# Kernel tuning notes

Hardware: AMD Instinct MI355X
Metric: run time of the kernel (lower is better)

The kernel has to match this reference:

```python
import jax, jax.numpy as jnp
import numpy as np

NEG_BIG = 1e13  # matches the torch module's (mask-1)*1e13 additive mask


def setup_inputs() -> dict:
    key = jax.random.key(0)
    k1, k2, k3, k4 = jax.random.split(key, 4)
    B, Lq, Lk, D = 32, 1024, 1024, 1024  # D = 2*hidden = 2*embedding
    query = jax.random.normal(k1, (B, Lq, D), dtype=jnp.float32)
    key_t = jax.random.normal(k2, (B, Lk, D), dtype=jnp.float32)
    key_mask = jax.random.randint(k3, (B, Lk), 0, 2).astype(jnp.float32)
    # Linear(hidden*2 -> embedding*2): weight [out, in] torch convention
    W = jax.random.normal(k4, (D, D), dtype=jnp.float32) * (1.0 / np.sqrt(D))
    b = jnp.zeros((D,), dtype=jnp.float32)
    return {"query": query, "key": key_t, "key_mask": key_mask, "W": W, "b": b}


def reference(query, key, key_mask, W, b):
    # query_emb: Dropout (identity at eval) -> Linear -> ReLU
    query_feat = jax.nn.relu(jnp.einsum("bqd,ed->bqe", query, W) + b)  # [B,Lq,D]
    # bmm with multiplicatively masked key
    masked_key = key * key_mask[:, :, None]                             # [B,Lk,D]
    score = jnp.einsum("bqd,bkd->bqk", query_feat, masked_key)          # [B,Lq,Lk]
    # masked_softmax: score*mask + (mask-1)*1e13, softmax over last dim
    m = key_mask[:, None, :]                                            # [B,1,Lk]
    attn = jax.nn.softmax(score * m + (m - 1.0) * NEG_BIG, axis=-1)     # [B,Lq,Lk]
    # weighted sum over the UNmasked key (as in the original module)
    return jnp.einsum("bqk,bkd->bqd", attn, key)                        # [B,Lq,D]
```

## Files before the change

### kernel.cpp

```cpp
#include <hip/hip_runtime.h>
#include <hip/hip_bf16.h>


typedef __attribute__((ext_vector_type(4))) float f32x4;
typedef __attribute__((ext_vector_type(8))) short s16x8;

#define MFMA16(a, b, c) __builtin_amdgcn_mfma_f32_16x16x32_bf16((a), (b), (c), 0, 0, 0)

__device__ __forceinline__ unsigned short f2bf(float x) {
  unsigned u = __builtin_bit_cast(unsigned, x);
  return (unsigned short)((u + 0x7FFFu + ((u >> 16) & 1u)) >> 16);
}
__device__ __forceinline__ float bf2f(unsigned short h) {
  return __builtin_bit_cast(float, ((unsigned)h) << 16);
}
__device__ __forceinline__ int swz(int row, int col) {
  return (row * 64 + col) ^ ((row & 7) << 3);
}
__device__ __forceinline__ void cvt8(const float* __restrict__ s, s16x8& h8, s16x8& l8) {
  f32x4 a = *(const f32x4*)s;
  f32x4 b = *(const f32x4*)(s + 4);
#pragma unroll
  for (int i = 0; i < 8; i++) {
    float v = (i < 4) ? a[i] : b[i - 4];
    unsigned short hu = f2bf(v);
    unsigned short lu = f2bf(v - bf2f(hu));
    h8[i] = (short)hu;
    l8[i] = (short)lu;
  }
}
__device__ __forceinline__ void gld16(const void* g, void* lds) {
  __builtin_amdgcn_global_load_lds((const __attribute__((address_space(1))) unsigned int*)g,
                                   (__attribute__((address_space(3))) unsigned int*)lds, 16, 0, 0);
}

#define OFF_KHI 0ULL
#define OFF_KLO 67108864ULL
#define OFF_KHIT 134217728ULL
#define OFF_QHI 201326592ULL
#define OFF_QLO 268435456ULL
#define OFF_WHI 335544320ULL
#define OFF_WLO 337641472ULL
#define WS_TIER_A 339738624ULL
#define QA_LO 33554432ULL

__global__ __launch_bounds__(256) void k_cvt_qw(const float* __restrict__ Q,
                                                unsigned short* __restrict__ Qhi,
                                                unsigned short* __restrict__ Qlo,
                                                const float* __restrict__ W,
                                                unsigned short* __restrict__ Whi,
                                                unsigned short* __restrict__ Wlo) {
  int i = blockIdx.x * 256 + threadIdx.x;
  s16x8 h, l;
  if (i < 4194304) {
    cvt8(Q + (size_t)i * 8, h, l);
    *(s16x8*)(Qhi + (size_t)i * 8) = h;
    *(s16x8*)(Qlo + (size_t)i * 8) = l;
  } else {
    int j = i - 4194304;
    if (j < 131072) {
      cvt8(W + (size_t)j * 8, h, l);
      *(s16x8*)(Whi + (size_t)j * 8) = h;
      *(s16x8*)(Wlo + (size_t)j * 8) = l;
    }
  }
}

__global__ __launch_bounds__(256) void k_cvt_k(const float* __restrict__ K,
                                               unsigned short* __restrict__ Khi,
                                               unsigned short* __restrict__ Klo,
                                               unsigned short* __restrict__ KhiT) {
  __shared__ unsigned T[64 * 65];
  const int t = threadIdx.x;
  const int db0 = blockIdx.x * 64, kb0 = blockIdx.y * 64, b = blockIdx.z;
  const size_t base = (size_t)b * 1024 * 1024;
#pragma unroll
  for (int i = 0; i < 2; i++) {
    const int r = (t >> 3) + i * 32, c0 = (t & 7) * 8;
    s16x8 h, l;
    cvt8(K + base + (size_t)(kb0 + r) * 1024 + db0 + c0, h, l);
    *(s16x8*)(Khi + base + (size_t)(kb0 + r) * 1024 + db0 + c0) = h;
    *(s16x8*)(Klo + base + (size_t)(kb0 + r) * 1024 + db0 + c0) = l;
#pragma unroll
    for (int j = 0; j < 8; j++)
      T[r * 65 + c0 + j] = ((unsigned)(unsigned short)h[j] << 16) | (unsigned short)l[j];
  }
  __syncthreads();
#pragma unroll
  for (int i = 0; i < 2; i++) {
    const int rd = (t >> 3) + i * 32, ck0 = (t & 7) * 8;
    s16x8 h;
#pragma unroll
    for (int j = 0; j < 8; j++) h[j] = (short)(unsigned short)(T[(ck0 + j) * 65 + rd] >> 16);
    *(s16x8*)(KhiT + base + (size_t)(db0 + rd) * 1024 + kb0 + ck0) = h;
  }
}

__global__ __launch_bounds__(256, 2) void k_qf2(const unsigned short* __restrict__ Qhi,
                                                const unsigned short* __restrict__ Qlo,
                                                const unsigned short* __restrict__ Whi,
                                                const unsigned short* __restrict__ Wlo,
                                                const float* __restrict__ bias,
                                                float* __restrict__ outp) {
  __shared__ __align__(16) unsigned short Ah[128 * 64], Al[128 * 64], Bh[128 * 64], Bl[128 * 64];
  const int t = threadIdx.x;
  const int i = blockIdx.x + blockIdx.y * 256;
  const int x = i & 7, j = i >> 3;
  const int n0 = (j & 7) * 128;
  const int m0 = (x * 32 + (j >> 3)) * 128;
  const int w = t >> 6, l = t & 63, wm = w >> 1, wn = w & 1, g = l >> 4, ln = l & 15;
  const int lrow = l >> 3, lc8 = (l & 7) * 8;
  const f32x4 fz = {0.f, 0.f, 0.f, 0.f};
  f32x4 acc[4][4];
#pragma unroll
  for (int a = 0; a < 4; a++)
#pragma unroll
    for (int bq = 0; bq < 4; bq++) acc[a][bq] = fz;
#pragma unroll 1
  for (int k0 = 0; k0 < 1024; k0 += 64) {
#pragma unroll
    for (int jj = 0; jj < 4; jj++) {
      const int ch = w * 4 + jj;
      const int row = ch * 8 + lrow;
      const int sc = lc8 ^ (lrow << 3);
      gld16(Qhi + (size_t)(m0 + row) * 1024 + k0 + sc, &Ah[ch * 512]);
      gld16(Qlo + (size_t)(m0 + row) * 1024 + k0 + sc, &Al[ch * 512]);
      gld16(Whi + (size_t)(n0 + row) * 1024 + k0 + sc, &Bh[ch * 512]);
      gld16(Wlo + (size_t)(n0 + row) * 1024 + k0 + sc, &Bl[ch * 512]);
    }
    __syncthreads();
#pragma unroll
    for (int ks = 0; ks < 2; ks++) {
      const int kc = ks * 32 + g * 8;
      s16x8 ah[4], al[4], bh[4], bl[4];
#pragma unroll
      for (int mf = 0; mf < 4; mf++) {
        const int row = wm * 64 + mf * 16 + ln;
        const int idx = row * 64 + (kc ^ ((row & 7) << 3));
        ah[mf] = *(const s16x8*)&Ah[idx];
        al[mf] = *(const s16x8*)&Al[idx];
      }
#pragma unroll
      for (int nf = 0; nf < 4; nf++) {
        const int row = wn * 64 + nf * 16 + ln;
        const int idx = row * 64 + (kc ^ ((row & 7) << 3));
        bh[nf] = *(const s16x8*)&Bh[idx];
        bl[nf] = *(const s16x8*)&Bl[idx];
      }
#pragma unroll
      for (int mf = 0; mf < 4; mf++)
#pragma unroll
        for (int nf = 0; nf < 4; nf++) {
          acc[mf][nf] = MFMA16(ah[mf], bh[nf], acc[mf][nf]);
          acc[mf][nf] = MFMA16(ah[mf], bl[nf], acc[mf][nf]);
          acc[mf][nf] = MFMA16(al[mf], bh[nf], acc[mf][nf]);
        }
    }
    __syncthreads();
  }
  unsigned short* qA = (unsigned short*)outp;
#pragma unroll
  for (int nf = 0; nf < 4; nf++) {
    const int c = n0 + wn * 64 + nf * 16 + ln;
    const float bv = bias[c];
    const int kchunk = c >> 5, lhib = ((c >> 3) & 3) << 4, jj = c & 7;
#pragma unroll
    for (int mf = 0; mf < 4; mf++)
#pragma unroll
      for (int r = 0; r < 4; r++) {
        const int R = m0 + wm * 64 + mf * 16 + g * 4 + r;
        float v = acc[mf][nf][r] + bv;
        v = v > 0.f ? v : 0.f;
        unsigned short h = f2bf(v);
        const size_t fo = (((size_t)(R >> 4) * 32 + kchunk) * 64 + ((R & 15) + lhib)) * 8 + jj;
        qA[fo] = h;
        qA[QA_LO + fo] = f2bf(v - bf2f(h));
      }
  }
}

__global__ __launch_bounds__(512, 2) void k_attn2(const unsigned short* __restrict__ Khi,
                                                  const unsigned short* __restrict__ Klo,
                                                  const float* __restrict__ mask,
                                                  const unsigned short* __restrict__ qA,
                                                  unsigned short* __restrict__ attnw) {
  __shared__ __align__(16) unsigned short kbuf[2][2][128 * 64];
  __shared__ float mask_s[1024];
  __shared__ float red[4][64];
  const int t = threadIdx.x;
  const int i = blockIdx.y * 16 + blockIdx.x;
  const int x = i & 7, jj = i >> 3;
  const int b = x * 4 + (jj >> 4), qt = jj & 15;
  const int q0 = qt * 64;
  const int w = t >> 6, l = t & 63, wm = w >> 2, wn = w & 3, g = l >> 4, ln = l & 15;
  const int lrow = l >> 3, lc8 = (l & 7) * 8, sc = lc8 ^ (lrow << 3);
  for (int ii = t; ii < 1024; ii += 512) mask_s[ii] = mask[b * 1024 + ii];
  const f32x4 fz = {0.f, 0.f, 0.f, 0.f};
  f32x4 acc[8][2][2];
#pragma unroll
  for (int kt = 0; kt < 8; kt++)
#pragma unroll
    for (int mf = 0; mf < 2; mf++)
#pragma unroll
      for (int nf = 0; nf < 2; nf++) acc[kt][mf][nf] = fz;
  const size_t kbase = (size_t)b * 1024 * 1024;
  const int qblk0 = (b * 1024 + q0) >> 4;

  auto stageK = [&](int buf, int kt, int dc) {
#pragma unroll
    for (int jj2 = 0; jj2 < 2; jj2++) {
      const int ch = w * 2 + jj2;
      const int row = ch * 8 + lrow;
      const size_t go = kbase + (size_t)(kt * 128 + row) * 1024 + dc * 64 + sc;
      gld16(Khi + go, &kbuf[buf][0][ch * 512]);
      gld16(Klo + go, &kbuf[buf][1][ch * 512]);
    }
  };

  stageK(0, 0, 0);
  __syncthreads();
#pragma unroll 1
  for (int dc = 0; dc < 16; dc++) {
    s16x8 qh[2][2], ql[2][2];
#pragma unroll
    for (int mf = 0; mf < 2; mf++) {
      const int qb = qblk0 + wm * 2 + mf;
#pragma unroll
      for (int ks = 0; ks < 2; ks++) {
        const size_t fo = (((size_t)qb * 32 + dc * 2 + ks) * 64 + l) * 8;
        qh[mf][ks] = *(const s16x8*)(qA + fo);
        ql[mf][ks] = *(const s16x8*)(qA + QA_LO + fo);
      }
    }
#pragma unroll
    for (int kt = 0; kt < 8; kt++) {
      const int snum = dc * 8 + kt;
      if (snum == 127) {
        asm volatile("s_waitcnt vmcnt(0)" ::: "memory");
      } else if (kt == 0) {
        asm volatile("s_waitcnt vmcnt(8)" ::: "memory");
      } else {
        asm volatile("s_waitcnt vmcnt(4)" ::: "memory");
      }
      __builtin_amdgcn_s_barrier();
      __builtin_amdgcn_sched_barrier(0);
      if (snum < 127) {
        const int nkt = (kt + 1) & 7;
        const int ndc = (kt == 7) ? dc + 1 : dc;
        stageK((snum + 1) & 1, nkt, ndc);
      }
      const int cur = snum & 1;
      __builtin_amdgcn_s_setprio(1);
#pragma unroll
      for (int ks = 0; ks < 2; ks++) {
        const int kc = ks * 32 + g * 8;
        s16x8 bh[2], bl[2];
#pragma unroll
        for (int nf = 0; nf < 2; nf++) {
          const int row = wn * 32 + nf * 16 + ln;
          const int idx = row * 64 + (kc ^ ((row & 7) << 3));
          bh[nf] = *(const s16x8*)&kbuf[cur][0][idx];
          bl[nf] = *(const s16x8*)&kbuf[cur][1][idx];
        }
#pragma unroll
        for (int mf = 0; mf < 2; mf++)
#pragma unroll
          for (int nf = 0; nf < 2; nf++) {
            acc[kt][mf][nf] = MFMA16(qh[mf][ks], bh[nf], acc[kt][mf][nf]);
            acc[kt][mf][nf] = MFMA16(qh[mf][ks], bl[nf], acc[kt][mf][nf]);
            acc[kt][mf][nf] = MFMA16(ql[mf][ks], bh[nf], acc[kt][mf][nf]);
          }
      }
      __builtin_amdgcn_s_setprio(0);
    }
  }
  __syncthreads();
  float rmax[2][4];
#pragma unroll
  for (int mf = 0; mf < 2; mf++)
#pragma unroll
    for (int r = 0; r < 4; r++) rmax[mf][r] = -1e30f;
#pragma unroll
  for (int kt = 0; kt < 8; kt++)
#pragma unroll
    for (int nf = 0; nf < 2; nf++) {
      const int k = kt * 128 + wn * 32 + nf * 16 + ln;
      const bool mk = mask_s[k] != 0.f;
#pragma unroll
      for (int mf = 0; mf < 2; mf++)
#pragma unroll
        for (int r = 0; r < 4; r++)
          if (mk) rmax[mf][r] = fmaxf(rmax[mf][r], acc[kt][mf][nf][r]);
    }
#pragma unroll
  for (int off = 1; off < 16; off <<= 1)
#pragma unroll
    for (int mf = 0; mf < 2; mf++)
#pragma unroll
      for (int r = 0; r < 4; r++) rmax[mf][r] = fmaxf(rmax[mf][r], __shfl_xor(rmax[mf][r], off));
  if (ln == 0) {
#pragma unroll
    for (int mf = 0; mf < 2; mf++)
#pragma unroll
      for (int r = 0; r < 4; r++) red[wn][wm * 32 + mf * 16 + g * 4 + r] = rmax[mf][r];
  }
  __syncthreads();
#pragma unroll
  for (int mf = 0; mf < 2; mf++)
#pragma unroll
    for (int r = 0; r < 4; r++) {
      const int row = wm * 32 + mf * 16 + g * 4 + r;
      rmax[mf][r] = fmaxf(fmaxf(red[0][row], red[1][row]), fmaxf(red[2][row], red[3][row]));
    }
  __syncthreads();
  float rsum[2][4];
#pragma unroll
  for (int mf = 0; mf < 2; mf++)
#pragma unroll
    for (int r = 0; r < 4; r++) rsum[mf][r] = 0.f;
#pragma unroll
  for (int kt = 0; kt < 8; kt++)
#pragma unroll
    for (int nf = 0; nf < 2; nf++) {
      const int k = kt * 128 + wn * 32 + nf * 16 + ln;
      const bool mk = mask_s[k] != 0.f;
#pragma unroll
      for (int mf = 0; mf < 2; mf++)
#pragma unroll
        for (int r = 0; r < 4; r++)
          if (mk) rsum[mf][r] += __expf(acc[kt][mf][nf][r] - rmax[mf][r]);
    }
#pragma unroll
  for (int off = 1; off < 16; off <<= 1)
#pragma unroll
    for (int mf = 0; mf < 2; mf++)
#pragma unroll
      for (int r = 0; r < 4; r++) rsum[mf][r] += __shfl_xor(rsum[mf][r], off);
  if (ln == 0) {
#pragma unroll
    for (int mf = 0; mf < 2; mf++)
#pragma unroll
      for (int r = 0; r < 4; r++) red[wn][wm * 32 + mf * 16 + g * 4 + r] = rsum[mf][r];
  }
  __syncthreads();
  float rinv[2][4];
#pragma unroll
  for (int mf = 0; mf < 2; mf++)
#pragma unroll
    for (int r = 0; r < 4; r++) {
      const int row = wm * 32 + mf * 16 + g * 4 + r;
      rinv[mf][r] = 1.f / (red[0][row] + red[1][row] + red[2][row] + red[3][row]);
    }
#pragma unroll
  for (int kt = 0; kt < 8; kt++)
#pragma unroll
    for (int nf = 0; nf < 2; nf++) {
      const int k = kt * 128 + wn * 32 + nf * 16 + ln;
      const bool mk = mask_s[k] != 0.f;
#pragma unroll
      for (int mf = 0; mf < 2; mf++)
#pragma unroll
        for (int r = 0; r < 4; r++) {
          const int q = q0 + wm * 32 + mf * 16 + g * 4 + r;
          float p = mk ? __expf(acc[kt][mf][nf][r] - rmax[mf][r]) * rinv[mf][r] : 0.f;
          attnw[(size_t)(b * 1024 + q) * 1024 + k] = f2bf(p);
        }
    }
}

__global__ __launch_bounds__(512, 1) void k_pv2(const unsigned short* __restrict__ KhiT,
                                                const unsigned short* __restrict__ attnw,
                                                float* __restrict__ dout) {
  __shared__ __align__(16) unsigned short Pb[2][128 * 64];
  __shared__ __align__(16) unsigned short KTb[2][512 * 64];
  const int t = threadIdx.x;
  const int i = blockIdx.y * 8 + blockIdx.x;
  const int x = i & 7, jj = i >> 3;
  const int b = x * 4 + (jj >> 3), qt = jj & 7;
  const int q0 = qt * 128, d0 = blockIdx.z * 512;
  const int w = t >> 6, l = t & 63, wm = w >> 2, wd = w & 3, g = l >> 4, ln = l & 15;
  const int lrow = l >> 3, lc8 = (l & 7) * 8, sc = lc8 ^ (lrow << 3);
  const f32x4 fz = {0.f, 0.f, 0.f, 0.f};
  f32x4 acc[4][8];
#pragma unroll
  for (int a = 0; a < 4; a++)
#pragma unroll
    for (int bq = 0; bq < 8; bq++) acc[a][bq] = fz;
  const size_t kbase = (size_t)b * 1024 * 1024;

  auto stageP = [&](int buf, int k0) {
#pragma unroll
    for (int jj2 = 0; jj2 < 2; jj2++) {
      const int ch = w * 2 + jj2;
      const int row = ch * 8 + lrow;
      gld16(attnw + (size_t)(b * 1024 + q0 + row) * 1024 + k0 + sc, &Pb[buf][ch * 512]);
    }
  };
  auto stageKT = [&](int buf, int k0) {
#pragma unroll
    for (int jj2 = 0; jj2 < 8; jj2++) {
      const int ch = w * 8 + jj2;
      const int row = ch * 8 + lrow;
      gld16(KhiT + kbase + (size_t)(d0 + row) * 1024 + k0 + sc, &KTb[buf][ch * 512]);
    }
  };

  stageP(0, 0);
  stageKT(0, 0);
#pragma unroll 1
  for (int s = 0; s < 16; s++) {
    asm volatile("s_waitcnt vmcnt(0)" ::: "memory");
    __builtin_amdgcn_s_barrier();
    __builtin_amdgcn_sched_barrier(0);
    if (s < 15) {
      stageP((s + 1) & 1, (s + 1) * 64);
      stageKT((s + 1) & 1, (s + 1) * 64);
    }
    const int cur = s & 1;
    __builtin_amdgcn_s_setprio(1);
#pragma unroll
    for (int ks = 0; ks < 2; ks++) {
      const int kc = ks * 32 + g * 8;
      s16x8 a[4], bb[8];
#pragma unroll
      for (int mf = 0; mf < 4; mf++) {
        const int row = wm * 64 + mf * 16 + ln;
        a[mf] = *(const s16x8*)&Pb[cur][row * 64 + (kc ^ ((row & 7) << 3))];
      }
#pragma unroll
      for (int nf = 0; nf < 8; nf++) {
        const int row = wd * 128 + nf * 16 + ln;
        bb[nf] = *(const s16x8*)&KTb[cur][row * 64 + (kc ^ ((row & 7) << 3))];
      }
#pragma unroll
      for (int mf = 0; mf < 4; mf++)
#pragma unroll
        for (int nf = 0; nf < 8; nf++) acc[mf][nf] = MFMA16(a[mf], bb[nf], acc[mf][nf]);
    }
    __builtin_amdgcn_s_setprio(0);
  }
#pragma unroll
  for (int mf = 0; mf < 4; mf++)
#pragma unroll
    for (int nf = 0; nf < 8; nf++)
#pragma unroll
      for (int r = 0; r < 4; r++) {
        const int q = q0 + wm * 64 + mf * 16 + g * 4 + r;
        const int d = d0 + wd * 128 + nf * 16 + ln;
        dout[(size_t)(b * 1024 + q) * 1024 + d] = acc[mf][nf][r];
      }
}

__global__ __launch_bounds__(256, 2) void k_qf(const float* __restrict__ Q,
                                               const float* __restrict__ W,
                                               const float* __restrict__ bias,
                                               float* __restrict__ qf) {
  __shared__ __align__(16) short Ah[128 * 64], Al[128 * 64], Bh[128 * 64], Bl[128 * 64];
  const int t = threadIdx.x;
  const int m0 = blockIdx.x * 128, n0 = blockIdx.y * 128;
  const int w = t >> 6, l = t & 63, wm = w >> 1, wn = w & 1, g = l >> 4, ln = l & 15;
  const f32x4 fz = {0.f, 0.f, 0.f, 0.f};
  f32x4 acc[4][4];
#pragma unroll
  for (int a = 0; a < 4; a++)
#pragma unroll
    for (int bq = 0; bq < 4; bq++) acc[a][bq] = fz;
  const int srow = t >> 1, scol = (t & 1) * 32;
#pragma unroll 1
  for (int k0 = 0; k0 < 1024; k0 += 64) {
    const float* sa = Q + (size_t)(m0 + srow) * 1024 + k0 + scol;
    const float* sb = W + (size_t)(n0 + srow) * 1024 + k0 + scol;
#pragma unroll
    for (int c = 0; c < 32; c += 8) {
      s16x8 h, lo;
      cvt8(sa + c, h, lo);
      int si = swz(srow, scol + c);
      *(s16x8*)&Ah[si] = h;
      *(s16x8*)&Al[si] = lo;
    }
#pragma unroll
    for (int c = 0; c < 32; c += 8) {
      s16x8 h, lo;
      cvt8(sb + c, h, lo);
      int si = swz(srow, scol + c);
      *(s16x8*)&Bh[si] = h;
      *(s16x8*)&Bl[si] = lo;
    }
    __syncthreads();
#pragma unroll
    for (int ks = 0; ks < 2; ks++) {
      const int kc = ks * 32 + g * 8;
      s16x8 ah[4], al[4], bh[4], bl[4];
#pragma unroll
      for (int mf = 0; mf < 4; mf++) {
        int si = swz(wm * 64 + mf * 16 + ln, kc);
        ah[mf] = *(s16x8*)&Ah[si];
        al[mf] = *(s16x8*)&Al[si];
      }
#pragma unroll
      for (int nf = 0; nf < 4; nf++) {
        int si = swz(wn * 64 + nf * 16 + ln, kc);
        bh[nf] = *(s16x8*)&Bh[si];
        bl[nf] = *(s16x8*)&Bl[si];
      }
#pragma unroll
      for (int mf = 0; mf < 4; mf++)
#pragma unroll
        for (int nf = 0; nf < 4; nf++) {
          acc[mf][nf] = MFMA16(ah[mf], bh[nf], acc[mf][nf]);
          acc[mf][nf] = MFMA16(ah[mf], bl[nf], acc[mf][nf]);
          acc[mf][nf] = MFMA16(al[mf], bh[nf], acc[mf][nf]);
        }
    }
    __syncthreads();
  }
#pragma unroll
  for (int nf = 0; nf < 4; nf++) {
    const int col = n0 + wn * 64 + nf * 16 + ln;
    const float bv = bias[col];
#pragma unroll
    for (int mf = 0; mf < 4; mf++)
#pragma unroll
      for (int r = 0; r < 4; r++) {
        const int row = m0 + wm * 64 + mf * 16 + g * 4 + r;
        float v = acc[mf][nf][r] + bv;
        qf[(size_t)row * 1024 + col] = v > 0.f ? v : 0.f;
      }
  }
}

__global__ __launch_bounds__(512, 2) void k_attn(const float* __restrict__ Key,
                                                 const float* __restrict__ mask,
                                                 float* __restrict__ dout) {
  __shared__ __align__(16) short qh[64 * 64], qlo[64 * 64], kh[128 * 64], klo[128 * 64];
  __shared__ float mask_s[1024];
  __shared__ float red[4][64];
  const int t = threadIdx.x;
  const int qt = blockIdx.x, b = blockIdx.y;
  const int q0 = qt * 64;
  const int w = t >> 6, l = t & 63, wm = w >> 2, wn = w & 3, g = l >> 4, ln = l & 15;
  for (int i = t; i < 1024; i += 512) mask_s[i] = mask[b * 1024 + i];
  const f32x4 fz = {0.f, 0.f, 0.f, 0.f};
  f32x4 acc[8][2][2];
#pragma unroll
  for (int kt = 0; kt < 8; kt++)
#pragma unroll
    for (int mf = 0; mf < 2; mf++)
#pragma unroll
      for (int nf = 0; nf < 2; nf++) acc[kt][mf][nf] = fz;
  const float* qfb = dout + (size_t)(b * 1024 + q0) * 1024;
  const float* kb = Key + (size_t)b * 1024 * 1024;
  const int qrow = t >> 3, qcol = (t & 7) * 8;
  const int krow = t >> 2, kcol0 = (t & 3) * 16;
#pragma unroll 1
  for (int dc = 0; dc < 16; dc++) {
    {
      s16x8 h, lo;
      cvt8(qfb + (size_t)qrow * 1024 + dc * 64 + qcol, h, lo);
      int si = swz(qrow, qcol);
      *(s16x8*)&qh[si] = h;
      *(s16x8*)&qlo[si] = lo;
    }
#pragma unroll
    for (int kt = 0; kt < 8; kt++) {
      {
        const float* s = kb + (size_t)(kt * 128 + krow) * 1024 + dc * 64 + kcol0;
        s16x8 h, lo;
        cvt8(s, h, lo);
        int si = swz(krow, kcol0);
        *(s16x8*)&kh[si] = h;
        *(s16x8*)&klo[si] = lo;
        cvt8(s + 8, h, lo);
        si = swz(krow, kcol0 + 8);
        *(s16x8*)&kh[si] = h;
        *(s16x8*)&klo[si] = lo;
      }
      __syncthreads();
#pragma unroll
      for (int ks = 0; ks < 2; ks++) {
        const int kc = ks * 32 + g * 8;
        s16x8 ah[2], al2[2], bh[2], bl[2];
#pragma unroll
        for (int mf = 0; mf < 2; mf++) {
          int si = swz(wm * 32 + mf * 16 + ln, kc);
          ah[mf] = *(s16x8*)&qh[si];
          al2[mf] = *(s16x8*)&qlo[si];
        }
#pragma unroll
        for (int nf = 0; nf < 2; nf++) {
          int si = swz(wn * 32 + nf * 16 + ln, kc);
          bh[nf] = *(s16x8*)&kh[si];
          bl[nf] = *(s16x8*)&klo[si];
        }
#pragma unroll
        for (int mf = 0; mf < 2; mf++)
#pragma unroll
          for (int nf = 0; nf < 2; nf++) {
            acc[kt][mf][nf] = MFMA16(ah[mf], bh[nf], acc[kt][mf][nf]);
            acc[kt][mf][nf] = MFMA16(ah[mf], bl[nf], acc[kt][mf][nf]);
            acc[kt][mf][nf] = MFMA16(al2[mf], bh[nf], acc[kt][mf][nf]);
          }
      }
      __syncthreads();
    }
  }
  float rmax[2][4];
#pragma unroll
  for (int mf = 0; mf < 2; mf++)
#pragma unroll
    for (int r = 0; r < 4; r++) rmax[mf][r] = -1e30f;
#pragma unroll
  for (int kt = 0; kt < 8; kt++)
#pragma unroll
    for (int nf = 0; nf < 2; nf++) {
      const int k = kt * 128 + wn * 32 + nf * 16 + ln;
      const bool mk = mask_s[k] != 0.f;
#pragma unroll
      for (int mf = 0; mf < 2; mf++)
#pragma unroll
        for (int r = 0; r < 4; r++)
          if (mk) rmax[mf][r] = fmaxf(rmax[mf][r], acc[kt][mf][nf][r]);
    }
#pragma unroll
  for (int off = 1; off < 16; off <<= 1)
#pragma unroll
    for (int mf = 0; mf < 2; mf++)
#pragma unroll
      for (int r = 0; r < 4; r++) rmax[mf][r] = fmaxf(rmax[mf][r], __shfl_xor(rmax[mf][r], off));
  if (ln == 0) {
#pragma unroll
    for (int mf = 0; mf < 2; mf++)
#pragma unroll
      for (int r = 0; r < 4; r++) red[wn][wm * 32 + mf * 16 + g * 4 + r] = rmax[mf][r];
  }
  __syncthreads();
#pragma unroll
  for (int mf = 0; mf < 2; mf++)
#pragma unroll
    for (int r = 0; r < 4; r++) {
      const int row = wm * 32 + mf * 16 + g * 4 + r;
      rmax[mf][r] = fmaxf(fmaxf(red[0][row], red[1][row]), fmaxf(red[2][row], red[3][row]));
    }
  __syncthreads();
  float rsum[2][4];
#pragma unroll
  for (int mf = 0; mf < 2; mf++)
#pragma unroll
    for (int r = 0; r < 4; r++) rsum[mf][r] = 0.f;
#pragma unroll
  for (int kt = 0; kt < 8; kt++)
#pragma unroll
    for (int nf = 0; nf < 2; nf++) {
      const int k = kt * 128 + wn * 32 + nf * 16 + ln;
      const bool mk = mask_s[k] != 0.f;
#pragma unroll
      for (int mf = 0; mf < 2; mf++)
#pragma unroll
        for (int r = 0; r < 4; r++)
          if (mk) rsum[mf][r] += __expf(acc[kt][mf][nf][r] - rmax[mf][r]);
    }
#pragma unroll
  for (int off = 1; off < 16; off <<= 1)
#pragma unroll
    for (int mf = 0; mf < 2; mf++)
#pragma unroll
      for (int r = 0; r < 4; r++) rsum[mf][r] += __shfl_xor(rsum[mf][r], off);
  if (ln == 0) {
#pragma unroll
    for (int mf = 0; mf < 2; mf++)
#pragma unroll
      for (int r = 0; r < 4; r++) red[wn][wm * 32 + mf * 16 + g * 4 + r] = rsum[mf][r];
  }
  __syncthreads();
  float rinv[2][4];
#pragma unroll
  for (int mf = 0; mf < 2; mf++)
#pragma unroll
    for (int r = 0; r < 4; r++) {
      const int row = wm * 32 + mf * 16 + g * 4 + r;
      rinv[mf][r] = 1.f / (red[0][row] + red[1][row] + red[2][row] + red[3][row]);
    }
  char* oc = (char*)dout;
#pragma unroll
  for (int kt = 0; kt < 8; kt++)
#pragma unroll
    for (int nf = 0; nf < 2; nf++) {
      const int k = kt * 128 + wn * 32 + nf * 16 + ln;
      const bool mk = mask_s[k] != 0.f;
#pragma unroll
      for (int mf = 0; mf < 2; mf++)
#pragma unroll
        for (int r = 0; r < 4; r++) {
          const int q = q0 + wm * 32 + mf * 16 + g * 4 + r;
          float p = mk ? __expf(acc[kt][mf][nf][r] - rmax[mf][r]) * rinv[mf][r] : 0.f;
          *(unsigned short*)(oc + (size_t)(b * 1024 + q) * 4096 + 2048 + k * 2) = f2bf(p);
        }
    }
}

__global__ __launch_bounds__(512, 2) void k_pv(const float* __restrict__ Key,
                                               float* __restrict__ dout, const int dh) {
  __shared__ __align__(16) short P[128 * 64];
  __shared__ __align__(16) short KT[512 * 64];
  const int t = threadIdx.x;
  const int qt = blockIdx.x, b = blockIdx.y;
  const int q0 = qt * 128, d0 = dh * 512;
  const int w = t >> 6, l = t & 63, wm = w >> 2, wd = w & 3, g = l >> 4, ln = l & 15;
  const f32x4 fz = {0.f, 0.f, 0.f, 0.f};
  f32x4 acc[4][8];
#pragma unroll
  for (int a = 0; a < 4; a++)
#pragma unroll
    for (int bq = 0; bq < 8; bq++) acc[a][bq] = fz;
  const char* ab = (const char*)dout;
  const int prow = t >> 2, pc0 = (t & 3) * 16;
#pragma unroll 1
  for (int k0 = 0; k0 < 1024; k0 += 64) {
    {
      const unsigned short* s =
          (const unsigned short*)(ab + (size_t)(b * 1024 + q0 + prow) * 4096 + 2048) + k0 + pc0;
      s16x8 p0 = *(const s16x8*)s, p1 = *(const s16x8*)(s + 8);
      *(s16x8*)&P[swz(prow, pc0)] = p0;
      *(s16x8*)&P[swz(prow, pc0 + 8)] = p1;
    }
    {
      const float* ksrc = Key + (size_t)b * 1024 * 1024 + (size_t)k0 * 1024 + d0 + t;
#pragma unroll
      for (int kg = 0; kg < 8; kg++) {
        s16x8 h;
#pragma unroll
        for (int jx = 0; jx < 8; jx++) h[jx] = (short)f2bf(ksrc[(size_t)(kg * 8 + jx) * 1024]);
        *(s16x8*)&KT[swz(t, kg * 8)] = h;
      }
    }
    __syncthreads();
#pragma unroll
    for (int ks = 0; ks < 2; ks++) {
      const int kc = ks * 32 + g * 8;
      s16x8 a[4], bb[8];
#pragma unroll
      for (int mf = 0; mf < 4; mf++) a[mf] = *(s16x8*)&P[swz(wm * 64 + mf * 16 + ln, kc)];
#pragma unroll
      for (int nf = 0; nf < 8; nf++) bb[nf] = *(s16x8*)&KT[swz(wd * 128 + nf * 16 + ln, kc)];
#pragma unroll
      for (int mf = 0; mf < 4; mf++)
#pragma unroll
        for (int nf = 0; nf < 8; nf++) acc[mf][nf] = MFMA16(a[mf], bb[nf], acc[mf][nf]);
    }
    __syncthreads();
  }
#pragma unroll
  for (int mf = 0; mf < 4; mf++)
#pragma unroll
    for (int nf = 0; nf < 8; nf++)
#pragma unroll
      for (int r = 0; r < 4; r++) {
        const int q = q0 + wm * 64 + mf * 16 + g * 4 + r;
        const int d = d0 + wd * 128 + nf * 16 + ln;
        dout[(size_t)(b * 1024 + q) * 1024 + d] = acc[mf][nf][r];
      }
}

extern "C" void kernel_launch(void* const* d_in, const int* in_sizes, int n_in,
                              void* d_out, int out_size, void* d_ws, size_t ws_size,
                              hipStream_t stream) {
  const float* Q = (const float*)d_in[0];
  const float* K = (const float*)d_in[1];
  const float* M = (const float*)d_in[2];
  const float* W = (const float*)d_in[3];
  const float* bias = (const float*)d_in[4];
  float* out = (float*)d_out;
  char* wsb = (char*)d_ws;
  (void)in_sizes; (void)n_in; (void)out_size;

  if (ws_size >= WS_TIER_A) {
    unsigned short* Khi = (unsigned short*)(wsb + OFF_KHI);
    unsigned short* Klo = (unsigned short*)(wsb + OFF_KLO);
    unsigned short* KhiT = (unsigned short*)(wsb + OFF_KHIT);
    unsigned short* Qhi = (unsigned short*)(wsb + OFF_QHI);
    unsigned short* Qlo = (unsigned short*)(wsb + OFF_QLO);
    unsigned short* Whi = (unsigned short*)(wsb + OFF_WHI);
    unsigned short* Wlo = (unsigned short*)(wsb + OFF_WLO);
    unsigned short* attnw = Qhi;
    k_cvt_k<<<dim3(16, 16, 32), 256, 0, stream>>>(K, Khi, Klo, KhiT);
    k_cvt_qw<<<16896, 256, 0, stream>>>(Q, Qhi, Qlo, W, Whi, Wlo);
    k_qf2<<<dim3(256, 8), 256, 0, stream>>>(Qhi, Qlo, Whi, Wlo, bias, out);
    k_attn2<<<dim3(16, 32), 512, 0, stream>>>(Khi, Klo, M, (const unsigned short*)out, attnw);
    k_pv2<<<dim3(8, 32, 2), 512, 0, stream>>>(KhiT, attnw, out);
  } else {
    k_qf<<<dim3(256, 8), 256, 0, stream>>>(Q, W, bias, out);
    k_attn<<<dim3(16, 32), 512, 0, stream>>>(K, M, out);
    k_pv<<<dim3(8, 32), 512, 0, stream>>>(K, out, 0);
    k_pv<<<dim3(8, 32), 512, 0, stream>>>(K, out, 1);
  }
}
```

Measured before the change: 722.3 us.

## Split fused score+softmax kernel into tiled score GEMM and separate softmax kernel

Replaces the fused k_attn2 kernel, which held a full 64x1024 score row block in registers and ran softmax in place, with two kernels. The first is a 128x128-tiled GEMM (k_sgemm) that writes split hi/lo bf16 scores to workspace. The second is a row-wise softmax kernel that reads the scores back and writes bf16 probabilities. The aim is to lift occupancy and tile parallelism in the score GEMM and to drop the large register accumulator, at the cost of an extra round trip of the score matrix through global memory. The new GEMM also loses the old double-buffered K staging and synchronises twice per d-chunk.

```diff
diff --git a/kernel.cpp b/kernel.cpp
--- a/kernel.cpp
+++ b/kernel.cpp
@@ -4,6 +4,7 @@
 
 typedef __attribute__((ext_vector_type(4))) float f32x4;
 typedef __attribute__((ext_vector_type(8))) short s16x8;
+typedef __attribute__((ext_vector_type(4))) short s16x4;
 
 #define MFMA16(a, b, c) __builtin_amdgcn_mfma_f32_16x16x32_bf16((a), (b), (c), 0, 0, 0)
 
@@ -179,193 +180,128 @@
   }
 }
 
-__global__ __launch_bounds__(512, 2) void k_attn2(const unsigned short* __restrict__ Khi,
+__global__ __launch_bounds__(256, 3) void k_sgemm(const unsigned short* __restrict__ Khi,
                                                   const unsigned short* __restrict__ Klo,
-                                                  const float* __restrict__ mask,
                                                   const unsigned short* __restrict__ qA,
-                                                  unsigned short* __restrict__ attnw) {
-  __shared__ __align__(16) unsigned short kbuf[2][2][128 * 64];
-  __shared__ float mask_s[1024];
-  __shared__ float red[4][64];
+                                                  unsigned short* __restrict__ Shi,
+                                                  unsigned short* __restrict__ Slo) {
+  __shared__ __align__(16) unsigned short Bh[128 * 64], Bl[128 * 64];
   const int t = threadIdx.x;
-  const int i = blockIdx.y * 16 + blockIdx.x;
+  const int i = blockIdx.x;
   const int x = i & 7, jj = i >> 3;
-  const int b = x * 4 + (jj >> 4), qt = jj & 15;
-  const int q0 = qt * 64;
-  const int w = t >> 6, l = t & 63, wm = w >> 2, wn = w & 3, g = l >> 4, ln = l & 15;
+  const int b = x * 4 + (jj >> 6);
+  const int r2 = jj & 63, qt = r2 >> 3, kt = r2 & 7;
+  const int q0 = b * 1024 + qt * 128;
+  const int k0g = kt * 128;
+  const int w = t >> 6, l = t & 63, wm = w >> 1, wn = w & 1, g = l >> 4, ln = l & 15;
   const int lrow = l >> 3, lc8 = (l & 7) * 8, sc = lc8 ^ (lrow << 3);
-  for (int ii = t; ii < 1024; ii += 512) mask_s[ii] = mask[b * 1024 + ii];
+  const size_t kbase = (size_t)b * 1024 * 1024;
+  const int qb0 = q0 >> 4;
   const f32x4 fz = {0.f, 0.f, 0.f, 0.f};
-  f32x4 acc[8][2][2];
-#pragma unroll
-  for (int kt = 0; kt < 8; kt++)
-#pragma unroll
-    for (int mf = 0; mf < 2; mf++)
-#pragma unroll
-      for (int nf = 0; nf < 2; nf++) acc[kt][mf][nf] = fz;
-  const size_t kbase = (size_t)b * 1024 * 1024;
-  const int qblk0 = (b * 1024 + q0) >> 4;
-
-  auto stageK = [&](int buf, int kt, int dc) {
-#pragma unroll
-    for (int jj2 = 0; jj2 < 2; jj2++) {
-      const int ch = w * 2 + jj2;
-      const int row = ch * 8 + lrow;
-      const size_t go = kbase + (size_t)(kt * 128 + row) * 1024 + dc * 64 + sc;
-      gld16(Khi + go, &kbuf[buf][0][ch * 512]);
-      gld16(Klo + go, &kbuf[buf][1][ch * 512]);
-    }
-  };
-
-  stageK(0, 0, 0);
-  __syncthreads();
+  f32x4 acc[4][4];
+#pragma unroll
+  for (int a = 0; a < 4; a++)
+#pragma unroll
+    for (int bq = 0; bq < 4; bq++) acc[a][bq] = fz;
 #pragma unroll 1
   for (int dc = 0; dc < 16; dc++) {
-    s16x8 qh[2][2], ql[2][2];
-#pragma unroll
-    for (int mf = 0; mf < 2; mf++) {
-      const int qb = qblk0 + wm * 2 + mf;
-#pragma unroll
-      for (int ks = 0; ks < 2; ks++) {
-        const size_t fo = (((size_t)qb * 32 + dc * 2 + ks) * 64 + l) * 8;
-        qh[mf][ks] = *(const s16x8*)(qA + fo);
-        ql[mf][ks] = *(const s16x8*)(qA + QA_LO + fo);
-      }
-    }
-#pragma unroll
-    for (int kt = 0; kt < 8; kt++) {
-      const int snum = dc * 8 + kt;
-      if (snum == 127) {
-        asm volatile("s_waitcnt vmcnt(0)" ::: "memory");
-      } else if (kt == 0) {
-        asm volatile("s_waitcnt vmcnt(8)" ::: "memory");
-      } else {
-        asm volatile("s_waitcnt vmcnt(4)" ::: "memory");
-      }
-      __builtin_amdgcn_s_barrier();
-      __builtin_amdgcn_sched_barrier(0);
-      if (snum < 127) {
-        const int nkt = (kt + 1) & 7;
-        const int ndc = (kt == 7) ? dc + 1 : dc;
-        stageK((snum + 1) & 1, nkt, ndc);
-      }
-      const int cur = snum & 1;
-      __builtin_amdgcn_s_setprio(1);
-#pragma unroll
-      for (int ks = 0; ks < 2; ks++) {
-        const int kc = ks * 32 + g * 8;
-        s16x8 bh[2], bl[2];
-#pragma unroll
-        for (int nf = 0; nf < 2; nf++) {
-          const int row = wn * 32 + nf * 16 + ln;
-          const int idx = row * 64 + (kc ^ ((row & 7) << 3));
-          bh[nf] = *(const s16x8*)&kbuf[cur][0][idx];
-          bl[nf] = *(const s16x8*)&kbuf[cur][1][idx];
+#pragma unroll
+    for (int jj2 = 0; jj2 < 4; jj2++) {
+      const int ch = w * 4 + jj2;
+      const int row = ch * 8 + lrow;
+      const size_t go = kbase + (size_t)(k0g + row) * 1024 + dc * 64 + sc;
+      gld16(Khi + go, &Bh[ch * 512]);
+      gld16(Klo + go, &Bl[ch * 512]);
+    }
+    __syncthreads();
+#pragma unroll
+    for (int ks = 0; ks < 2; ks++) {
+      s16x8 ah[4], al[4], bh[4], bl[4];
+#pragma unroll
+      for (int mf = 0; mf < 4; mf++) {
+        const size_t fo = (((size_t)(qb0 + wm * 4 + mf) * 32 + dc * 2 + ks) * 64 + l) * 8;
+        ah[mf] = *(const s16x8*)(qA + fo);
+        al[mf] = *(const s16x8*)(qA + QA_LO + fo);
+      }
+      const int kc = ks * 32 + g * 8;
+#pragma unroll
+      for (int nf = 0; nf < 4; nf++) {
+        const int row = wn * 64 + nf * 16 + ln;
+        const int idx = row * 64 + (kc ^ ((row & 7) << 3));
+        bh[nf] = *(const s16x8*)&Bh[idx];
+        bl[nf] = *(const s16x8*)&Bl[idx];
+      }
+#pragma unroll
+      for (int mf = 0; mf < 4; mf++)
+#pragma unroll
+        for (int nf = 0; nf < 4; nf++) {
+          acc[mf][nf] = MFMA16(ah[mf], bh[nf], acc[mf][nf]);
+          acc[mf][nf] = MFMA16(ah[mf], bl[nf], acc[mf][nf]);
+          acc[mf][nf] = MFMA16(al[mf], bh[nf], acc[mf][nf]);
         }
-#pragma unroll
-        for (int mf = 0; mf < 2; mf++)
-#pragma unroll
-          for (int nf = 0; nf < 2; nf++) {
-            acc[kt][mf][nf] = MFMA16(qh[mf][ks], bh[nf], acc[kt][mf][nf]);
-            acc[kt][mf][nf] = MFMA16(qh[mf][ks], bl[nf], acc[kt][mf][nf]);
-            acc[kt][mf][nf] = MFMA16(ql[mf][ks], bh[nf], acc[kt][mf][nf]);
-          }
-      }
-      __builtin_amdgcn_s_setprio(0);
-    }
-  }
+    }
+    __syncthreads();
+  }
+#pragma unroll
+  for (int mf = 0; mf < 4; mf++)
+#pragma unroll
+    for (int nf = 0; nf < 4; nf++) {
+      const int colS = k0g + wn * 64 + nf * 16 + ln;
+#pragma unroll
+      for (int r = 0; r < 4; r++) {
+        const int rowS = q0 + wm * 64 + mf * 16 + g * 4 + r;
+        const float v = acc[mf][nf][r];
+        const unsigned short h = f2bf(v);
+        Shi[(size_t)rowS * 1024 + colS] = h;
+        Slo[(size_t)rowS * 1024 + colS] = f2bf(v - bf2f(h));
+      }
+    }
+}
+
+__global__ __launch_bounds__(256) void k_softmax(const unsigned short* __restrict__ Shi,
+                                                 const unsigned short* __restrict__ Slo,
+                                                 const float* __restrict__ mask,
+                                                 unsigned short* __restrict__ P) {
+  __shared__ float red[2][4];
+  const int row = blockIdx.x;
+  const int b = row >> 10;
+  const int t = threadIdx.x, w = t >> 6, l = t & 63;
+  const size_t base = (size_t)row * 1024 + t * 4;
+  const s16x4 hi = *(const s16x4*)(Shi + base);
+  const s16x4 lo = *(const s16x4*)(Slo + base);
+  const f32x4 mk = *(const f32x4*)(mask + b * 1024 + t * 4);
+  float s[4];
+  bool um[4];
+#pragma unroll
+  for (int j = 0; j < 4; j++) {
+    s[j] = bf2f((unsigned short)hi[j]) + bf2f((unsigned short)lo[j]);
+    um[j] = mk[j] != 0.f;
+  }
+  float mx = -1e30f;
+#pragma unroll
+  for (int j = 0; j < 4; j++)
+    if (um[j]) mx = fmaxf(mx, s[j]);
+#pragma unroll
+  for (int off = 1; off < 64; off <<= 1) mx = fmaxf(mx, __shfl_xor(mx, off));
+  if (l == 0) red[0][w] = mx;
   __syncthreads();
-  float rmax[2][4];
-#pragma unroll
-  for (int mf = 0; mf < 2; mf++)
-#pragma unroll
-    for (int r = 0; r < 4; r++) rmax[mf][r] = -1e30f;
-#pragma unroll
-  for (int kt = 0; kt < 8; kt++)
-#pragma unroll
-    for (int nf = 0; nf < 2; nf++) {
-      const int k = kt * 128 + wn * 32 + nf * 16 + ln;
-      const bool mk = mask_s[k] != 0.f;
-#pragma unroll
-      for (int mf = 0; mf < 2; mf++)
-#pragma unroll
-        for (int r = 0; r < 4; r++)
-          if (mk) rmax[mf][r] = fmaxf(rmax[mf][r], acc[kt][mf][nf][r]);
-    }
-#pragma unroll
-  for (int off = 1; off < 16; off <<= 1)
-#pragma unroll
-    for (int mf = 0; mf < 2; mf++)
-#pragma unroll
-      for (int r = 0; r < 4; r++) rmax[mf][r] = fmaxf(rmax[mf][r], __shfl_xor(rmax[mf][r], off));
-  if (ln == 0) {
-#pragma unroll
-    for (int mf = 0; mf < 2; mf++)
-#pragma unroll
-      for (int r = 0; r < 4; r++) red[wn][wm * 32 + mf * 16 + g * 4 + r] = rmax[mf][r];
-  }
+  mx = fmaxf(fmaxf(red[0][0], red[0][1]), fmaxf(red[0][2], red[0][3]));
+  float e[4];
+  float sum = 0.f;
+#pragma unroll
+  for (int j = 0; j < 4; j++) {
+    e[j] = um[j] ? __expf(s[j] - mx) : 0.f;
+    sum += e[j];
+  }
+#pragma unroll
+  for (int off = 1; off < 64; off <<= 1) sum += __shfl_xor(sum, off);
+  if (l == 0) red[1][w] = sum;
   __syncthreads();
-#pragma unroll
-  for (int mf = 0; mf < 2; mf++)
-#pragma unroll
-    for (int r = 0; r < 4; r++) {
-      const int row = wm * 32 + mf * 16 + g * 4 + r;
-      rmax[mf][r] = fmaxf(fmaxf(red[0][row], red[1][row]), fmaxf(red[2][row], red[3][row]));
-    }
-  __syncthreads();
-  float rsum[2][4];
-#pragma unroll
-  for (int mf = 0; mf < 2; mf++)
-#pragma unroll
-    for (int r = 0; r < 4; r++) rsum[mf][r] = 0.f;
-#pragma unroll
-  for (int kt = 0; kt < 8; kt++)
-#pragma unroll
-    for (int nf = 0; nf < 2; nf++) {
-      const int k = kt * 128 + wn * 32 + nf * 16 + ln;
-      const bool mk = mask_s[k] != 0.f;
-#pragma unroll
-      for (int mf = 0; mf < 2; mf++)
-#pragma unroll
-        for (int r = 0; r < 4; r++)
-          if (mk) rsum[mf][r] += __expf(acc[kt][mf][nf][r] - rmax[mf][r]);
-    }
-#pragma unroll
-  for (int off = 1; off < 16; off <<= 1)
-#pragma unroll
-    for (int mf = 0; mf < 2; mf++)
-#pragma unroll
-      for (int r = 0; r < 4; r++) rsum[mf][r] += __shfl_xor(rsum[mf][r], off);
-  if (ln == 0) {
-#pragma unroll
-    for (int mf = 0; mf < 2; mf++)
-#pragma unroll
-      for (int r = 0; r < 4; r++) red[wn][wm * 32 + mf * 16 + g * 4 + r] = rsum[mf][r];
-  }
-  __syncthreads();
-  float rinv[2][4];
-#pragma unroll
-  for (int mf = 0; mf < 2; mf++)
-#pragma unroll
-    for (int r = 0; r < 4; r++) {
-      const int row = wm * 32 + mf * 16 + g * 4 + r;
-      rinv[mf][r] = 1.f / (red[0][row] + red[1][row] + red[2][row] + red[3][row]);
-    }
-#pragma unroll
-  for (int kt = 0; kt < 8; kt++)
-#pragma unroll
-    for (int nf = 0; nf < 2; nf++) {
-      const int k = kt * 128 + wn * 32 + nf * 16 + ln;
-      const bool mk = mask_s[k] != 0.f;
-#pragma unroll
-      for (int mf = 0; mf < 2; mf++)
-#pragma unroll
-        for (int r = 0; r < 4; r++) {
-          const int q = q0 + wm * 32 + mf * 16 + g * 4 + r;
-          float p = mk ? __expf(acc[kt][mf][nf][r] - rmax[mf][r]) * rinv[mf][r] : 0.f;
-          attnw[(size_t)(b * 1024 + q) * 1024 + k] = f2bf(p);
-        }
-    }
+  const float rinv = 1.f / (red[1][0] + red[1][1] + red[1][2] + red[1][3]);
+  s16x4 o;
+#pragma unroll
+  for (int j = 0; j < 4; j++) o[j] = (short)f2bf(e[j] * rinv);
+  *(s16x4*)(P + base) = o;
 }
 
 __global__ __launch_bounds__(512, 1) void k_pv2(const unsigned short* __restrict__ KhiT,
@@ -781,12 +717,15 @@
     unsigned short* Qlo = (unsigned short*)(wsb + OFF_QLO);
     unsigned short* Whi = (unsigned short*)(wsb + OFF_WHI);
     unsigned short* Wlo = (unsigned short*)(wsb + OFF_WLO);
-    unsigned short* attnw = Qhi;
+    unsigned short* Shi = Qhi;
+    unsigned short* Slo = Qlo;
+    unsigned short* Pw = Klo;
     k_cvt_k<<<dim3(16, 16, 32), 256, 0, stream>>>(K, Khi, Klo, KhiT);
     k_cvt_qw<<<16896, 256, 0, stream>>>(Q, Qhi, Qlo, W, Whi, Wlo);
     k_qf2<<<dim3(256, 8), 256, 0, stream>>>(Qhi, Qlo, Whi, Wlo, bias, out);
-    k_attn2<<<dim3(16, 32), 512, 0, stream>>>(Khi, Klo, M, (const unsigned short*)out, attnw);
-    k_pv2<<<dim3(8, 32, 2), 512, 0, stream>>>(KhiT, attnw, out);
+    k_sgemm<<<2048, 256, 0, stream>>>(Khi, Klo, (const unsigned short*)out, Shi, Slo);
+    k_softmax<<<32768, 256, 0, stream>>>(Shi, Slo, M, Pw);
+    k_pv2<<<dim3(8, 32, 2), 512, 0, stream>>>(KhiT, Pw, out);
   } else {
     k_qf<<<dim3(256, 8), 256, 0, stream>>>(Q, W, bias, out);
     k_attn<<<dim3(16, 32), 512, 0, stream>>>(K, M, out);
```

New measurement: 724.3 us. About the same (+0.3%).
